# Kernel optimization log

Hardware: AMD Instinct MI355X
Metric: run time of the kernel (lower is better)

Reference implementation:

```python
import jax, jax.numpy as jnp
import numpy as np

N_NODES = 500000
IN_CH = 128
HID_CH = 128
NUM_GRAPHS = 1024


def setup_inputs() -> dict:
    key = jax.random.key(0)
    k1, k2, k3, k4, k5, k6 = jax.random.split(key, 6)
    x = jax.random.normal(k1, (N_NODES, IN_CH), dtype=jnp.float32)
    batch = jnp.sort(jax.random.randint(k2, (N_NODES,), 0, NUM_GRAPHS, dtype=jnp.int64))
    # Linear weights stored as [in, out] so forward is x @ W + b
    W1 = jax.random.normal(k3, (IN_CH, HID_CH), dtype=jnp.float32) / np.sqrt(IN_CH)
    b1 = jax.random.normal(k4, (HID_CH,), dtype=jnp.float32) * 0.01
    w2 = jax.random.normal(k5, (HID_CH,), dtype=jnp.float32) / np.sqrt(HID_CH)
    b2 = jax.random.normal(k6, (), dtype=jnp.float32) * 0.01
    return {"x": x, "batch": batch, "W1": W1, "b1": b1, "w2": w2, "b2": b2}


def reference(x, batch, W1, b1, w2, b2):
    # MLP attention scores: [N]
    h = jax.nn.relu(x @ W1 + b1)            # [N, H]
    scores = h @ w2 + b2                     # [N]
    # Segment-wise (per-graph) softmax, numerically stable
    seg_max = jax.ops.segment_max(scores, batch, num_segments=NUM_GRAPHS)
    e = jnp.exp(scores - seg_max[batch])     # [N]
    denom = jax.ops.segment_sum(e, batch, num_segments=NUM_GRAPHS)
    attn = e / denom[batch]                  # [N]
    # Weighted scatter-add pooling: [num_graphs, C]
    weighted = x * attn[:, None]
    return jax.ops.segment_sum(weighted, batch, num_segments=NUM_GRAPHS)
```

## Files before the change

kernel.cpp:

```cpp
#include <hip/hip_runtime.h>
#include <math.h>

#define NN 500000
#define CH 128
#define NG 1024
#define GRID_S 512
#define TILES ((NN + 127) >> 7)

typedef __attribute__((ext_vector_type(8))) short short8v;
typedef __attribute__((ext_vector_type(4))) float f32x4;

__device__ __forceinline__ void bf16_split(float f, unsigned short& h, unsigned short& l){
  const unsigned u = __float_as_uint(f);
  h = (unsigned short)(u >> 16);
  const float hif = __uint_as_float(u & 0xffff0000u);
  const float lof = f - hif;
  l = (unsigned short)(__float_as_uint(lof) >> 16);
}

__device__ __forceinline__ void gld_lds16(const void* g, void* l){
  __builtin_amdgcn_global_load_lds(
      (__attribute__((address_space(1))) void*)g,
      (__attribute__((address_space(3))) void*)l, 16, 0, 0);
}

__device__ __forceinline__ void cvt8(const float4 f0, const float4 f1,
                                     short8v& Ah, short8v& Al){
  float fv[8];
  *reinterpret_cast<float4*>(fv) = f0;
  *reinterpret_cast<float4*>(fv + 4) = f1;
  unsigned short hv[8], lv[8];
  #pragma unroll
  for (int j = 0; j < 8; j++) bf16_split(fv[j], hv[j], lv[j]);
  Ah = *reinterpret_cast<short8v*>(hv);
  Al = *reinterpret_cast<short8v*>(lv);
}

__global__ __launch_bounds__(256) void prep_kernel(
    const float* __restrict__ W1, unsigned short* __restrict__ Wg,
    const int* __restrict__ batch, int* __restrict__ start){
  const int t = blockIdx.x * 256 + threadIdx.x;
  if (t < 2048){
    const int n  = t >> 4;
    const int k0 = (t & 15) << 3;
    unsigned short hv[8], lv[8];
    #pragma unroll
    for (int i = 0; i < 8; i++)
      bf16_split(W1[(size_t)(k0 + i) * CH + n], hv[i], lv[i]);
    *reinterpret_cast<short8v*>(Wg + n * 128 + k0) = *reinterpret_cast<short8v*>(hv);
    *reinterpret_cast<short8v*>(Wg + 16384 + n * 128 + k0) = *reinterpret_cast<short8v*>(lv);
  } else if (t <= 2048 + NG){
    const int g = t - 2048;
    const bool is64 = (batch[NN - 1] == 0);
    if (g == NG){ start[NG] = NN; return; }
    int lo = 0, hi = NN;
    while (lo < hi){
      int mid = (lo + hi) >> 1;
      int v = is64 ? batch[2 * mid] : batch[mid];
      if (v < g) lo = mid + 1; else hi = mid;
    }
    start[g] = lo;
  }
}

__global__ __launch_bounds__(512, 4) void scores_mfma(
    const float* __restrict__ x, const unsigned short* __restrict__ Wg,
    const float* __restrict__ b1, const float* __restrict__ w2,
    const float* __restrict__ b2, float* __restrict__ escore)
{
  __shared__ char  XS[4 * 16384];
  __shared__ float p4[4][128];
  __shared__ float b1s[CH], w2s[CH];

  const int tid = threadIdx.x;
  const int w   = tid >> 6;
  const int l   = tid & 63;
  const int l15 = l & 15;
  const int g   = l >> 4;
  const int rw  = w & 1;
  const int cw  = w >> 1;

  const int bid = blockIdx.x;
  const int ntb = (TILES - 1 - bid) / GRID_S + 1;
  const int NP  = ntb * 4;
  const float b2v = b2[0];

  if (tid < CH){ b1s[tid] = b1[tid]; w2s[tid] = w2[tid]; }

  short8v Bf[2][4][2];
  #pragma unroll
  for (int ctk = 0; ctk < 2; ++ctk){
    const int n = (cw * 2 + ctk) * 16 + l15;
    #pragma unroll
    for (int kc = 0; kc < 4; ++kc){
      Bf[ctk][kc][0] = *reinterpret_cast<const short8v*>(Wg + n * 128 + kc * 32 + g * 8);
      Bf[ctk][kc][1] = *reinterpret_cast<const short8v*>(Wg + 16384 + n * 128 + kc * 32 + g * 8);
    }
  }

  int srcoff[2], dstoff[2];
  #pragma unroll
  for (int p = 0; p < 2; ++p){
    const int idx = p * 512 + tid;
    const int R = idx >> 3, c = idx & 7;
    srcoff[p] = R * 512 + ((c ^ (R & 7)) << 4);
    dstoff[p] = idx * 16;
  }
  auto stage = [&](int SL){
    char* base = XS + (SL & 3) * 16384;
    const size_t tb = (size_t)(bid + (SL >> 2) * GRID_S) * 65536 + (SL & 3) * 128;
    #pragma unroll
    for (int p = 0; p < 2; ++p){
      size_t so = tb + srcoff[p];
      if (so >= (size_t)NN * 512) so = (size_t)(NN - 1) * 512;
      gld_lds16((const char*)x + so, base + dstoff[p]);
    }
  };

  const int abase = (rw * 64 + l15) * 128;
  const int sw0 = ((2 * g)     ^ (l15 & 7)) << 4;
  const int sw1 = ((2 * g + 1) ^ (l15 & 7)) << 4;

  stage(0); stage(1);
  asm volatile("s_waitcnt vmcnt(0) lgkmcnt(0)" ::: "memory");
  __syncthreads();

  for (int ti = 0; ti < ntb; ++ti){
    const int tilebase = (bid + ti * GRID_S) * 128;

    f32x4 acc[4][2];
    #pragma unroll
    for (int a = 0; a < 4; ++a)
      #pragma unroll
      for (int b = 0; b < 2; ++b) acc[a][b] = (f32x4)0.f;

    #pragma unroll
    for (int ks = 0; ks < 4; ++ks){
      const int P = ti * 4 + ks;
      if (ti == ntb - 1 && ks == 3)
        asm volatile("s_waitcnt vmcnt(0)" ::: "memory");
      else if (ks <= 1 && w < 2 && ti > 0)
        asm volatile("s_waitcnt vmcnt(3)" ::: "memory");
      else
        asm volatile("s_waitcnt vmcnt(2)" ::: "memory");
      __builtin_amdgcn_s_barrier();
      if (P + 2 < NP) stage(P + 2);

      const char* sb = XS + ks * 16384;
      #pragma unroll
      for (int nt = 0; nt < 4; ++nt){
        const char* bp = sb + abase + nt * 2048;
        short8v Ah, Al;
        cvt8(*reinterpret_cast<const float4*>(bp + sw0),
             *reinterpret_cast<const float4*>(bp + sw1), Ah, Al);
        #pragma unroll
        for (int ctk = 0; ctk < 2; ++ctk){
          acc[nt][ctk] = __builtin_amdgcn_mfma_f32_16x16x32_bf16(Ah, Bf[ctk][ks][0], acc[nt][ctk], 0, 0, 0);
          acc[nt][ctk] = __builtin_amdgcn_mfma_f32_16x16x32_bf16(Al, Bf[ctk][ks][0], acc[nt][ctk], 0, 0, 0);
          acc[nt][ctk] = __builtin_amdgcn_mfma_f32_16x16x32_bf16(Ah, Bf[ctk][ks][1], acc[nt][ctk], 0, 0, 0);
        }
      }
    }

    const float b1v0 = b1s[cw * 32 + l15], b1v1 = b1s[cw * 32 + 16 + l15];
    const float w2v0 = w2s[cw * 32 + l15], w2v1 = w2s[cw * 32 + 16 + l15];
    #pragma unroll
    for (int nt = 0; nt < 4; ++nt){
      #pragma unroll
      for (int r = 0; r < 4; ++r){
        float s = fmaxf(acc[nt][0][r] + b1v0, 0.f) * w2v0;
        s = fmaf(fmaxf(acc[nt][1][r] + b1v1, 0.f), w2v1, s);
        s += __shfl_xor(s, 1); s += __shfl_xor(s, 2);
        s += __shfl_xor(s, 4); s += __shfl_xor(s, 8);
        if (l15 == 0) p4[cw][rw * 64 + nt * 16 + g * 4 + r] = s;
      }
    }
    asm volatile("s_waitcnt lgkmcnt(0)" ::: "memory");
    __builtin_amdgcn_s_barrier();
    if (tid < 128){
      const float s = p4[0][tid] + p4[1][tid] + p4[2][tid] + p4[3][tid] + b2v;
      const int grow = tilebase + tid;
      if (grow < NN) escore[grow] = __expf(s);
    }
  }
}

__global__ __launch_bounds__(512) void pool_kernel(
    const float* __restrict__ x, const float* __restrict__ es,
    const int* __restrict__ start, float* __restrict__ out){
  const int g = blockIdx.x;
  const int s0 = start[g], s1 = start[g + 1];
  const int tid = threadIdx.x;
  const int c4 = tid & 31;
  const int rg = tid >> 5;

  float4 a0 = make_float4(0.f, 0.f, 0.f, 0.f);
  float4 a1 = make_float4(0.f, 0.f, 0.f, 0.f);
  float d0 = 0.f, d1 = 0.f;
  int i = s0 + rg;
  for (; i + 16 < s1; i += 32){
    const float e0 = es[i];
    const float e1 = es[i + 16];
    const float4 v0 = reinterpret_cast<const float4*>(&x[(size_t)i * CH])[c4];
    const float4 v1 = reinterpret_cast<const float4*>(&x[(size_t)(i + 16) * CH])[c4];
    a0.x = fmaf(e0, v0.x, a0.x); a0.y = fmaf(e0, v0.y, a0.y);
    a0.z = fmaf(e0, v0.z, a0.z); a0.w = fmaf(e0, v0.w, a0.w);
    d0 += e0;
    a1.x = fmaf(e1, v1.x, a1.x); a1.y = fmaf(e1, v1.y, a1.y);
    a1.z = fmaf(e1, v1.z, a1.z); a1.w = fmaf(e1, v1.w, a1.w);
    d1 += e1;
  }
  if (i < s1){
    const float e0 = es[i];
    const float4 v0 = reinterpret_cast<const float4*>(&x[(size_t)i * CH])[c4];
    a0.x = fmaf(e0, v0.x, a0.x); a0.y = fmaf(e0, v0.y, a0.y);
    a0.z = fmaf(e0, v0.z, a0.z); a0.w = fmaf(e0, v0.w, a0.w);
    d0 += e0;
  }
  a0.x += a1.x; a0.y += a1.y; a0.z += a1.z; a0.w += a1.w;
  d0 += d1;

  __shared__ float4 red[16][32];
  __shared__ float redd[16][32];
  red[rg][c4] = a0;
  redd[rg][c4] = d0;
  __syncthreads();
  if (rg < 8){
    float4 o = red[rg + 8][c4], m = red[rg][c4];
    m.x += o.x; m.y += o.y; m.z += o.z; m.w += o.w;
    red[rg][c4] = m;
    redd[rg][c4] += redd[rg + 8][c4];
  }
  __syncthreads();
  if (rg < 4){
    float4 o = red[rg + 4][c4], m = red[rg][c4];
    m.x += o.x; m.y += o.y; m.z += o.z; m.w += o.w;
    red[rg][c4] = m;
    redd[rg][c4] += redd[rg + 4][c4];
  }
  __syncthreads();
  if (rg < 2){
    float4 o = red[rg + 2][c4], m = red[rg][c4];
    m.x += o.x; m.y += o.y; m.z += o.z; m.w += o.w;
    red[rg][c4] = m;
    redd[rg][c4] += redd[rg + 2][c4];
  }
  __syncthreads();
  if (rg == 0){
    float4 b0 = red[0][c4], b1v = red[1][c4];
    const float d = redd[0][c4] + redd[1][c4];
    const float inv = d > 0.f ? 1.f / d : 0.f;
    float4 r;
    r.x = (b0.x + b1v.x) * inv; r.y = (b0.y + b1v.y) * inv;
    r.z = (b0.z + b1v.z) * inv; r.w = (b0.w + b1v.w) * inv;
    reinterpret_cast<float4*>(&out[(size_t)g * CH])[c4] = r;
  }
}

extern "C" void kernel_launch(void* const* d_in, const int* in_sizes, int n_in,
                              void* d_out, int out_size, void* d_ws, size_t ws_size,
                              hipStream_t stream){
  const float* x    = (const float*)d_in[0];
  const int*   batch= (const int*)d_in[1];
  const float* W1   = (const float*)d_in[2];
  const float* b1   = (const float*)d_in[3];
  const float* w2   = (const float*)d_in[4];
  const float* b2   = (const float*)d_in[5];
  float* out = (float*)d_out;

  float* es    = (float*)d_ws;
  int*   start = (int*)((char*)d_ws + (size_t)NN * sizeof(float));
  unsigned short* Wg = (unsigned short*)((char*)d_ws + ((ws_size - 65536) & ~(size_t)255));

  prep_kernel<<<13, 256, 0, stream>>>(W1, Wg, batch, start);
  scores_mfma<<<GRID_S, 512, 0, stream>>>(x, Wg, b1, w2, b2, es);
  pool_kernel<<<NG, 512, 0, stream>>>(x, es, start, out);
}
```

Measured before the change: 138.8 us.

## Stage x through registers and split to bf16 once before writing LDS

Replaces the direct global-to-LDS async loads with register-staged global loads, double-buffered two k-steps ahead. Each thread converts its fp32 slice into bf16 hi/lo halves once and stores them to a half-size swizzled LDS buffer, so MFMA-feeding waves read ready-made bf16 fragments. Before, every wave redundantly re-split the same fp32 data it read from LDS. The cost is more VGPRs for staging and an LDS write plus barrier every k-step, which can reduce how well memory latency is hidden.

```diff
diff --git a/kernel.cpp b/kernel.cpp
--- a/kernel.cpp
+++ b/kernel.cpp
@@ -16,24 +16,6 @@
   const float hif = __uint_as_float(u & 0xffff0000u);
   const float lof = f - hif;
   l = (unsigned short)(__float_as_uint(lof) >> 16);
-}
-
-__device__ __forceinline__ void gld_lds16(const void* g, void* l){
-  __builtin_amdgcn_global_load_lds(
-      (__attribute__((address_space(1))) void*)g,
-      (__attribute__((address_space(3))) void*)l, 16, 0, 0);
-}
-
-__device__ __forceinline__ void cvt8(const float4 f0, const float4 f1,
-                                     short8v& Ah, short8v& Al){
-  float fv[8];
-  *reinterpret_cast<float4*>(fv) = f0;
-  *reinterpret_cast<float4*>(fv + 4) = f1;
-  unsigned short hv[8], lv[8];
-  #pragma unroll
-  for (int j = 0; j < 8; j++) bf16_split(fv[j], hv[j], lv[j]);
-  Ah = *reinterpret_cast<short8v*>(hv);
-  Al = *reinterpret_cast<short8v*>(lv);
 }
 
 __global__ __launch_bounds__(256) void prep_kernel(
@@ -68,7 +50,7 @@
     const float* __restrict__ b1, const float* __restrict__ w2,
     const float* __restrict__ b2, float* __restrict__ escore)
 {
-  __shared__ char  XS[4 * 16384];
+  __shared__ char  XS[2 * 16384];
   __shared__ float p4[4][128];
   __shared__ float b1s[CH], w2s[CH];
 
@@ -98,32 +80,22 @@
     }
   }
 
-  int srcoff[2], dstoff[2];
-  #pragma unroll
-  for (int p = 0; p < 2; ++p){
-    const int idx = p * 512 + tid;
-    const int R = idx >> 3, c = idx & 7;
-    srcoff[p] = R * 512 + ((c ^ (R & 7)) << 4);
-    dstoff[p] = idx * 16;
-  }
-  auto stage = [&](int SL){
-    char* base = XS + (SL & 3) * 16384;
-    const size_t tb = (size_t)(bid + (SL >> 2) * GRID_S) * 65536 + (SL & 3) * 128;
-    #pragma unroll
-    for (int p = 0; p < 2; ++p){
-      size_t so = tb + srcoff[p];
-      if (so >= (size_t)NN * 512) so = (size_t)(NN - 1) * 512;
-      gld_lds16((const char*)x + so, base + dstoff[p]);
-    }
+  const int Rs = tid >> 2, gw = tid & 3;
+  const int wbyte = Rs * 64 + ((gw ^ ((Rs >> 1) & 3)) << 4);
+  const int rbyte0 = (rw * 64 + l15) * 64 + (((g ^ ((l15 >> 1) & 3))) << 4);
+
+  auto issue = [&](float4* dst, int ti2, int ks2){
+    int row = (bid + ti2 * GRID_S) * 128 + Rs;
+    row = row < NN ? row : NN - 1;
+    const float4* src = reinterpret_cast<const float4*>(
+        (const char*)x + (size_t)row * 512 + ks2 * 128 + gw * 32);
+    dst[0] = src[0];
+    dst[1] = src[1];
   };
 
-  const int abase = (rw * 64 + l15) * 128;
-  const int sw0 = ((2 * g)     ^ (l15 & 7)) << 4;
-  const int sw1 = ((2 * g + 1) ^ (l15 & 7)) << 4;
-
-  stage(0); stage(1);
-  asm volatile("s_waitcnt vmcnt(0) lgkmcnt(0)" ::: "memory");
-  __syncthreads();
+  float4 stg[2][2];
+  issue(stg[0], 0, 0);
+  issue(stg[1], 0, 1);
 
   for (int ti = 0; ti < ntb; ++ti){
     const int tilebase = (bid + ti * GRID_S) * 128;
@@ -137,22 +109,36 @@
     #pragma unroll
     for (int ks = 0; ks < 4; ++ks){
       const int P = ti * 4 + ks;
-      if (ti == ntb - 1 && ks == 3)
-        asm volatile("s_waitcnt vmcnt(0)" ::: "memory");
-      else if (ks <= 1 && w < 2 && ti > 0)
-        asm volatile("s_waitcnt vmcnt(3)" ::: "memory");
-      else
-        asm volatile("s_waitcnt vmcnt(2)" ::: "memory");
+
+      {
+        float fv[8];
+        *reinterpret_cast<float4*>(fv)     = stg[ks & 1][0];
+        *reinterpret_cast<float4*>(fv + 4) = stg[ks & 1][1];
+        unsigned hq[4], lq[4];
+        #pragma unroll
+        for (int j = 0; j < 4; ++j){
+          const unsigned u0 = __float_as_uint(fv[2 * j]);
+          const unsigned u1 = __float_as_uint(fv[2 * j + 1]);
+          hq[j] = (u0 >> 16) | (u1 & 0xffff0000u);
+          const float l0 = fv[2 * j]     - __uint_as_float(u0 & 0xffff0000u);
+          const float l1 = fv[2 * j + 1] - __uint_as_float(u1 & 0xffff0000u);
+          lq[j] = (__float_as_uint(l0) >> 16) | (__float_as_uint(l1) & 0xffff0000u);
+        }
+        char* pane = XS + (ks & 1) * 16384;
+        *reinterpret_cast<uint4*>(pane + wbyte)        = make_uint4(hq[0], hq[1], hq[2], hq[3]);
+        *reinterpret_cast<uint4*>(pane + 8192 + wbyte) = make_uint4(lq[0], lq[1], lq[2], lq[3]);
+      }
+      if (P + 2 < NP) issue(stg[ks & 1], (P + 2) >> 2, (ks + 2) & 3);
+
+      asm volatile("s_waitcnt lgkmcnt(0)" ::: "memory");
       __builtin_amdgcn_s_barrier();
-      if (P + 2 < NP) stage(P + 2);
-
-      const char* sb = XS + ks * 16384;
+      asm volatile("" ::: "memory");
+
+      const char* ph = XS + (ks & 1) * 16384;
       #pragma unroll
       for (int nt = 0; nt < 4; ++nt){
-        const char* bp = sb + abase + nt * 2048;
-        short8v Ah, Al;
-        cvt8(*reinterpret_cast<const float4*>(bp + sw0),
-             *reinterpret_cast<const float4*>(bp + sw1), Ah, Al);
+        const short8v Ah = *reinterpret_cast<const short8v*>(ph + rbyte0 + nt * 1024);
+        const short8v Al = *reinterpret_cast<const short8v*>(ph + 8192 + rbyte0 + nt * 1024);
         #pragma unroll
         for (int ctk = 0; ctk < 2; ++ctk){
           acc[nt][ctk] = __builtin_amdgcn_mfma_f32_16x16x32_bf16(Ah, Bf[ctk][ks][0], acc[nt][ctk], 0, 0, 0);
@@ -177,6 +163,7 @@
     }
     asm volatile("s_waitcnt lgkmcnt(0)" ::: "memory");
     __builtin_amdgcn_s_barrier();
+    asm volatile("" ::: "memory");
     if (tid < 128){
       const float s = p4[0][tid] + p4[1][tid] + p4[2][tid] + p4[3][tid] + b2v;
       const int grow = tilebase + tid;
```

After: 133.7 us. 1.04x faster.
